# Optimization experiments

Measured on AMD Instinct MI355X. Metric: run time of the kernel, lower is better.

## Reference

```python
import jax, jax.numpy as jnp
import numpy as np

NEG_SLOPE = 0.2

def _gat_conv(x, src, dst, W, att_src, att_dst, bias, num_nodes):
    # x: [N, Fin], W: [H*C, Fin], att_*: [H, C], bias: [H*C]
    H, C = att_src.shape
    xh = (x @ W.T).reshape(num_nodes, H, C)            # [N,H,C]
    a_s = jnp.einsum('nhc,hc->nh', xh, att_src)         # [N,H]
    a_d = jnp.einsum('nhc,hc->nh', xh, att_dst)
    e = jax.nn.leaky_relu(a_s[src] + a_d[dst], NEG_SLOPE)  # [E,H]
    # segment softmax over destination node per head
    m = jax.ops.segment_max(e, dst, num_segments=num_nodes)      # [N,H]
    ex = jnp.exp(e - m[dst])
    s = jax.ops.segment_sum(ex, dst, num_segments=num_nodes)     # [N,H]
    alpha = ex / (s[dst] + 1e-16)                                # [E,H]
    msg = xh[src] * alpha[:, :, None]                            # [E,H,C]
    out = jax.ops.segment_sum(msg, dst, num_segments=num_nodes)  # [N,H,C]
    return out.reshape(num_nodes, H * C) + bias


def setup_inputs() -> dict:
    key = jax.random.key(0)
    ks = jax.random.split(key, 16)
    N, E, Fin, Hd, H1, G = 50000, 800000, 128, 128, 4, 128
    x = jax.random.normal(ks[0], (N, Fin), dtype=jnp.float32)
    edge_index = jax.random.randint(ks[1], (2, E), 0, N, dtype=jnp.int64)
    batch = jnp.sort(jax.random.randint(ks[2], (N,), 0, G, dtype=jnp.int64))
    sc1 = 1.0 / np.sqrt(Fin)
    sc2 = 1.0 / np.sqrt(Hd * H1)
    sch = 1.0 / np.sqrt(Hd)
    return {
        'x': x, 'edge_index': edge_index, 'batch': batch,
        'W1': jax.random.normal(ks[3], (Hd * H1, Fin), dtype=jnp.float32) * sc1,
        'as1': jax.random.normal(ks[4], (H1, Hd), dtype=jnp.float32) * 0.1,
        'ad1': jax.random.normal(ks[5], (H1, Hd), dtype=jnp.float32) * 0.1,
        'b1': jnp.zeros((Hd * H1,), dtype=jnp.float32),
        'W2': jax.random.normal(ks[6], (Hd, Hd * H1), dtype=jnp.float32) * sc2,
        'as2': jax.random.normal(ks[7], (1, Hd), dtype=jnp.float32) * 0.1,
        'ad2': jax.random.normal(ks[8], (1, Hd), dtype=jnp.float32) * 0.1,
        'b2': jnp.zeros((Hd,), dtype=jnp.float32),
        'Wh1': jax.random.normal(ks[9], (Hd, Hd), dtype=jnp.float32) * sch,
        'bh1': jnp.zeros((Hd,), dtype=jnp.float32),
        'Wh2': jax.random.normal(ks[10], (1, Hd), dtype=jnp.float32) * sch,
        'bh2': jnp.zeros((1,), dtype=jnp.float32),
    }


def reference(x, edge_index, batch, W1, as1, ad1, b1, W2, as2, ad2, b2, Wh1, bh1, Wh2, bh2):
    N = x.shape[0]
    G = 128  # num graphs
    # add self loops (PyG GATConv default)
    loops = jnp.arange(N, dtype=edge_index.dtype)
    src = jnp.concatenate([edge_index[0], loops])
    dst = jnp.concatenate([edge_index[1], loops])
    h = _gat_conv(x, src, dst, W1, as1, ad1, b1, N)   # [N, 512]
    h = jax.nn.elu(h)
    h = _gat_conv(h, src, dst, W2, as2, ad2, b2, N)   # [N, 128]
    h = jax.nn.elu(h)
    # global mean pool over batch
    sums = jax.ops.segment_sum(h, batch, num_segments=G)
    cnts = jax.ops.segment_sum(jnp.ones((N,), dtype=h.dtype), batch, num_segments=G)
    pooled = sums / jnp.maximum(cnts, 1.0)[:, None]   # [G, 128]
    z = jax.nn.relu(pooled @ Wh1.T + bh1)
    out = z @ Wh2.T + bh2                             # [G, 1]
    return out.reshape(-1)
```

## Files before the change

### kernel.cpp

```cpp
#include <hip/hip_runtime.h>
#include <cstdint>
#include <cstddef>

#define NEG_SLOPE 0.2f

typedef _Float16 f16x8 __attribute__((ext_vector_type(8)));
typedef _Float16 f16x2 __attribute__((ext_vector_type(2)));
typedef float    f32x4 __attribute__((ext_vector_type(4)));
typedef float    f32x2 __attribute__((ext_vector_type(2)));

__device__ __forceinline__ float leaky(float x){ return x > 0.f ? x : NEG_SLOPE * x; }
__device__ __forceinline__ float elu(float x){ return x > 0.f ? x : __expf(x) - 1.f; }

__global__ __launch_bounds__(256) void k_front(const float* __restrict__ W1,
                                               const float* __restrict__ W2,
                                               const float* __restrict__ as1,
                                               const float* __restrict__ ad1,
                                               _Float16* __restrict__ W1hi, _Float16* __restrict__ W1lo,
                                               _Float16* __restrict__ W2hi, _Float16* __restrict__ W2lo,
                                               float* __restrict__ w_s, float* __restrict__ w_d,
                                               const int* __restrict__ ei, int* __restrict__ deg,
                                               unsigned short* __restrict__ rank,
                                               const int* __restrict__ batch, int* __restrict__ gstart,
                                               int E, int Ep, int N, int G, int nbc)
{
    int b = blockIdx.x;
    if (b < 512) {
        const float* src = (b < 256) ? W1 : W2;
        _Float16* hi = (b < 256) ? W1hi : W2hi;
        _Float16* lo = (b < 256) ? W1lo : W2lo;
        int i = ((b & 255) << 8) + threadIdx.x;
        float v = src[i];
        _Float16 h = (_Float16)v;
        hi[i] = h;
        lo[i] = (_Float16)(v - (float)h);
    } else if (b < 514) {
        int h = (b - 512) * 2 + (threadIdx.x >> 7);
        int k = threadIdx.x & 127;
        float s = 0.f, d = 0.f;
        for (int c = 0; c < 128; ++c) {
            float w = W1[((size_t)(h * 128 + c)) * 128 + k];
            s += as1[h * 128 + c] * w;
            d += ad1[h * 128 + c] * w;
        }
        w_s[h * 128 + k] = s;
        w_d[h * 128 + k] = d;
    } else if (b < 514 + nbc) {
        int e = (b - 514) * 256 + threadIdx.x;
        if (e >= Ep) return;
        int dst = (e < E) ? ei[E + e] : (e - E);
        rank[e] = (unsigned short)atomicAdd(&deg[dst], 1);
    } else {
        int n = (b - 514 - nbc) * 256 + threadIdx.x;
        if (n >= N) return;
        int bb = batch[n];
        int prev = (n == 0) ? -1 : batch[n - 1];
        for (int g = prev + 1; g <= bb; ++g) gstart[g] = n;
        if (n == N - 1)
            for (int g = bb + 1; g <= G; ++g) gstart[g] = N;
    }
}

__global__ __launch_bounds__(1024) void k_scan_attn(const int* __restrict__ deg,
                                                    int* __restrict__ start,
                                                    int* __restrict__ sums,
                                                    int Ntot, int N, int nscan,
                                                    const float* __restrict__ x,
                                                    const float* __restrict__ w_s,
                                                    const float* __restrict__ w_d,
                                                    float* __restrict__ a_s,
                                                    float* __restrict__ a_d,
                                                    _Float16* __restrict__ xh)
{
    if ((int)blockIdx.x < nscan) {
        __shared__ int sm[1024];
        int tid = threadIdx.x;
        int i = blockIdx.x * 1024 + tid;
        int v = (i < N) ? deg[i] : 0;
        sm[tid] = v; __syncthreads();
        for (int off = 1; off < 1024; off <<= 1) {
            int t = (tid >= off) ? sm[tid - off] : 0;
            __syncthreads();
            sm[tid] += t;
            __syncthreads();
        }
        if (i < Ntot) start[i] = sm[tid] - v;
        if (tid == 1023) sums[blockIdx.x] = sm[1023];
    } else {
        int n = (blockIdx.x - nscan) * 16 + (threadIdx.x >> 6);
        if (n >= N) return;
        int lane = threadIdx.x & 63;
        float2 xv = *(const float2*)(x + (size_t)n * 128 + lane * 2);
        f16x2 hv = { (_Float16)xv.x, (_Float16)xv.y };
        *(f16x2*)(xh + (size_t)n * 128 + lane * 2) = hv;
        float ps[4], pd[4];
        #pragma unroll
        for (int h = 0; h < 4; ++h) {
            float2 sv = *(const float2*)(w_s + h * 128 + lane * 2);
            float2 dv = *(const float2*)(w_d + h * 128 + lane * 2);
            ps[h] = xv.x * sv.x + xv.y * sv.y;
            pd[h] = xv.x * dv.x + xv.y * dv.y;
        }
        #pragma unroll
        for (int h = 0; h < 4; ++h)
            for (int off = 32; off; off >>= 1) {
                ps[h] += __shfl_xor(ps[h], off);
                pd[h] += __shfl_xor(pd[h], off);
            }
        if (lane == 0) {
            *(float4*)(a_s + (size_t)n * 4) = make_float4(ps[0], ps[1], ps[2], ps[3]);
            *(float4*)(a_d + (size_t)n * 4) = make_float4(pd[0], pd[1], pd[2], pd[3]);
        }
    }
}

__global__ __launch_bounds__(1024) void k_scanC(int* __restrict__ start,
                                                const int* __restrict__ sums, int Ntot)
{
    int add = 0;
    for (int b = 0; b < (int)blockIdx.x; ++b) add += sums[b];
    int i = blockIdx.x * 1024 + threadIdx.x;
    if (i < Ntot) start[i] += add;
}

__global__ void k_fill(const int* __restrict__ ei, const int* __restrict__ start,
                       const unsigned short* __restrict__ rank,
                       unsigned short* __restrict__ csr_src, int E, int Ep)
{
    int e = blockIdx.x * blockDim.x + threadIdx.x;
    if (e >= Ep) return;
    int src, dst;
    if (e < E) { src = ei[e]; dst = ei[E + e]; } else { src = dst = e - E; }
    csr_src[start[dst] + rank[e]] = (unsigned short)src;
}

#define LSG 40
#define CP  136
__global__ __launch_bounds__(256, 2) void k_gemm12(
    const _Float16* __restrict__ agg,
    const _Float16* __restrict__ W1hi, const _Float16* __restrict__ W1lo,
    const float* __restrict__ b1,
    const _Float16* __restrict__ W2hi, const _Float16* __restrict__ W2lo,
    _Float16* __restrict__ xh2,
    const float* __restrict__ as2, const float* __restrict__ ad2,
    float* __restrict__ As2, float* __restrict__ Ad2, int M)
{
    __shared__ __align__(16) _Float16 smem[128 * LSG * 3 + 128 * CP];
    _Float16* As  = smem;
    _Float16* Bhs = smem + 128 * LSG;
    _Float16* Bls = smem + 256 * LSG;
    _Float16* Ct  = smem + 384 * LSG;

    const int tid = threadIdx.x;
    const int wave = tid >> 6, lane = tid & 63;
    const int wm = wave >> 1, wn = wave & 1;
    const int quad = lane >> 4, l16 = lane & 15;
    const int m0 = blockIdx.x * 128;

    f32x4 acc2[4][4] = {};

    for (int h = 0; h < 4; ++h) {
        f32x4 acc1[4][4] = {};
        for (int k0 = 0; k0 < 128; k0 += 32) {
            #pragma unroll
            for (int q = 0; q < 2; ++q) {
                int idx = tid + q * 256;
                int row = idx >> 2, kq = idx & 3;
                int rg = m0 + row;
                f16x8 va = {};
                if (rg < M) va = *(const f16x8*)(agg + (size_t)rg * 512 + h * 128 + k0 + kq * 8);
                *(f16x8*)&As[row * LSG + kq * 8] = va;
                size_t brow = (size_t)(h * 128 + row) * 128 + k0 + kq * 8;
                *(f16x8*)&Bhs[row * LSG + kq * 8] = *(const f16x8*)(W1hi + brow);
                *(f16x8*)&Bls[row * LSG + kq * 8] = *(const f16x8*)(W1lo + brow);
            }
            __syncthreads();
            f16x8 af[4], bhf[4], blf[4];
            #pragma unroll
            for (int i = 0; i < 4; ++i) {
                af[i]  = *(const f16x8*)&As [(wm * 64 + i * 16 + l16) * LSG + quad * 8];
                bhf[i] = *(const f16x8*)&Bhs[(wn * 64 + i * 16 + l16) * LSG + quad * 8];
                blf[i] = *(const f16x8*)&Bls[(wn * 64 + i * 16 + l16) * LSG + quad * 8];
            }
            #pragma unroll
            for (int i = 0; i < 4; ++i)
                #pragma unroll
                for (int j = 0; j < 4; ++j) {
                    acc1[i][j] = __builtin_amdgcn_mfma_f32_16x16x32_f16(af[i], bhf[j], acc1[i][j], 0, 0, 0);
                    acc1[i][j] = __builtin_amdgcn_mfma_f32_16x16x32_f16(af[i], blf[j], acc1[i][j], 0, 0, 0);
                }
            __syncthreads();
        }
        #pragma unroll
        for (int j = 0; j < 4; ++j) {
            int n = wn * 64 + j * 16 + l16;
            float bb = b1[h * 128 + n];
            #pragma unroll
            for (int i = 0; i < 4; ++i)
                #pragma unroll
                for (int r = 0; r < 4; ++r)
                    Ct[(wm * 64 + i * 16 + quad * 4 + r) * CP + n] = (_Float16)elu(acc1[i][j][r] + bb);
        }
        __syncthreads();
        for (int k0 = 0; k0 < 128; k0 += 32) {
            #pragma unroll
            for (int q = 0; q < 2; ++q) {
                int idx = tid + q * 256;
                int row = idx >> 2, kq = idx & 3;
                size_t brow = (size_t)row * 512 + h * 128 + k0 + kq * 8;
                *(f16x8*)&Bhs[row * LSG + kq * 8] = *(const f16x8*)(W2hi + brow);
                *(f16x8*)&Bls[row * LSG + kq * 8] = *(const f16x8*)(W2lo + brow);
            }
            __syncthreads();
            f16x8 af[4], bhf[4], blf[4];
            #pragma unroll
            for (int i = 0; i < 4; ++i) {
                af[i]  = *(const f16x8*)&Ct [(wm * 64 + i * 16 + l16) * CP + k0 + quad * 8];
                bhf[i] = *(const f16x8*)&Bhs[(wn * 64 + i * 16 + l16) * LSG + quad * 8];
                blf[i] = *(const f16x8*)&Bls[(wn * 64 + i * 16 + l16) * LSG + quad * 8];
            }
            #pragma unroll
            for (int i = 0; i < 4; ++i)
                #pragma unroll
                for (int j = 0; j < 4; ++j) {
                    acc2[i][j] = __builtin_amdgcn_mfma_f32_16x16x32_f16(af[i], bhf[j], acc2[i][j], 0, 0, 0);
                    acc2[i][j] = __builtin_amdgcn_mfma_f32_16x16x32_f16(af[i], blf[j], acc2[i][j], 0, 0, 0);
                }
            __syncthreads();
        }
    }

    #pragma unroll
    for (int j = 0; j < 4; ++j) {
        int n = wn * 64 + j * 16 + l16;
        #pragma unroll
        for (int i = 0; i < 4; ++i)
            #pragma unroll
            for (int r = 0; r < 4; ++r)
                Ct[(wm * 64 + i * 16 + quad * 4 + r) * CP + n] = (_Float16)acc2[i][j][r];
    }
    __syncthreads();
    for (int c = tid; c < 2048; c += 256) {
        int row = c >> 4, col8 = (c & 15) * 8;
        int m = m0 + row;
        if (m < M)
            *(f16x8*)(xh2 + (size_t)m * 128 + col8) = *(const f16x8*)&Ct[row * CP + col8];
    }
    {
        int row = tid >> 1, half = tid & 1;
        int d = m0 + row;
        float ss = 0.f, sd = 0.f;
        const _Float16* rp = &Ct[row * CP + half * 64];
        #pragma unroll
        for (int c8 = 0; c8 < 8; ++c8) {
            f16x8 v = *(const f16x8*)(rp + c8 * 8);
            #pragma unroll
            for (int c = 0; c < 8; ++c) {
                float f = (float)v[c];
                int n = half * 64 + c8 * 8 + c;
                ss += f * as2[n];
                sd += f * ad2[n];
            }
        }
        ss += __shfl_xor(ss, 1);
        sd += __shfl_xor(sd, 1);
        if (half == 0 && d < M) { As2[d] = ss; Ad2[d] = sd; }
    }
}

__global__ __launch_bounds__(256) void k_gat1(const int* __restrict__ start,
                                              const unsigned short* __restrict__ csr,
                                              const float* __restrict__ a_s,
                                              const float* __restrict__ a_d,
                                              const _Float16* __restrict__ x,
                                              _Float16* __restrict__ agg, int N)
{
    int d = blockIdx.x * 16 + (threadIdx.x >> 4);
    if (d >= N) return;
    int g16 = threadIdx.x & 15;
    int beg = start[d], end = start[d + 1];
    int deg = end - beg;
    float4 ad4 = *(const float4*)(a_d + (size_t)d * 4);

    float sum0 = 0.f, sum1 = 0.f, sum2 = 0.f, sum3 = 0.f;
    f32x2 acc[4][4] = {};
    const _Float16* xb = x + g16 * 8;

    for (int base = 0; base < deg; base += 16) {
        int nch = deg - base; if (nch > 16) nch = 16;
        int s = 0;
        float e0 = 0.f, e1 = 0.f, e2 = 0.f, e3 = 0.f;
        if (g16 < nch) {
            s = csr[beg + base + g16];
            float4 as4 = *(const float4*)(a_s + (size_t)s * 4);
            e0 = __expf(leaky(as4.x + ad4.x));
            e1 = __expf(leaky(as4.y + ad4.y));
            e2 = __expf(leaky(as4.z + ad4.z));
            e3 = __expf(leaky(as4.w + ad4.w));
            sum0 += e0; sum1 += e1; sum2 += e2; sum3 += e3;
        }
        int t = 0;
        for (; t + 8 <= nch; t += 8) {
            int si[8];
            #pragma unroll
            for (int u = 0; u < 8; ++u) si[u] = __shfl(s, t + u, 16);
            f16x8 hv[8];
            #pragma unroll
            for (int u = 0; u < 8; ++u) hv[u] = *(const f16x8*)(xb + (size_t)si[u] * 128);
            #pragma unroll
            for (int u = 0; u < 8; ++u) {
                float w0 = __shfl(e0, t + u, 16), w1 = __shfl(e1, t + u, 16);
                float w2 = __shfl(e2, t + u, 16), w3 = __shfl(e3, t + u, 16);
                #pragma unroll
                for (int p = 0; p < 4; ++p) {
                    f32x2 v = { (float)hv[u][2*p], (float)hv[u][2*p+1] };
                    acc[0][p] += w0 * v;
                    acc[1][p] += w1 * v;
                    acc[2][p] += w2 * v;
                    acc[3][p] += w3 * v;
                }
            }
        }
        for (; t + 4 <= nch; t += 4) {
            int sA = __shfl(s, t, 16),     sB = __shfl(s, t + 1, 16);
            int sC = __shfl(s, t + 2, 16), sD = __shfl(s, t + 3, 16);
            f16x8 hA = *(const f16x8*)(xb + (size_t)sA * 128);
            f16x8 hB = *(const f16x8*)(xb + (size_t)sB * 128);
            f16x8 hC = *(const f16x8*)(xb + (size_t)sC * 128);
            f16x8 hD = *(const f16x8*)(xb + (size_t)sD * 128);
            float w0A = __shfl(e0, t, 16),     w1A = __shfl(e1, t, 16);
            float w2A = __shfl(e2, t, 16),     w3A = __shfl(e3, t, 16);
            float w0B = __shfl(e0, t + 1, 16), w1B = __shfl(e1, t + 1, 16);
            float w2B = __shfl(e2, t + 1, 16), w3B = __shfl(e3, t + 1, 16);
            float w0C = __shfl(e0, t + 2, 16), w1C = __shfl(e1, t + 2, 16);
            float w2C = __shfl(e2, t + 2, 16), w3C = __shfl(e3, t + 2, 16);
            float w0D = __shfl(e0, t + 3, 16), w1D = __shfl(e1, t + 3, 16);
            float w2D = __shfl(e2, t + 3, 16), w3D = __shfl(e3, t + 3, 16);
            #pragma unroll
            for (int p = 0; p < 4; ++p) {
                f32x2 vA = { (float)hA[2*p], (float)hA[2*p+1] };
                f32x2 vB = { (float)hB[2*p], (float)hB[2*p+1] };
                f32x2 vC = { (float)hC[2*p], (float)hC[2*p+1] };
                f32x2 vD = { (float)hD[2*p], (float)hD[2*p+1] };
                acc[0][p] += w0A * vA + w0B * vB + w0C * vC + w0D * vD;
                acc[1][p] += w1A * vA + w1B * vB + w1C * vC + w1D * vD;
                acc[2][p] += w2A * vA + w2B * vB + w2C * vC + w2D * vD;
                acc[3][p] += w3A * vA + w3B * vB + w3C * vC + w3D * vD;
            }
        }
        for (; t < nch; ++t) {
            int   si = __shfl(s,  t, 16);
            float w0 = __shfl(e0, t, 16);
            float w1 = __shfl(e1, t, 16);
            float w2 = __shfl(e2, t, 16);
            float w3 = __shfl(e3, t, 16);
            f16x8 hv = *(const f16x8*)(xb + (size_t)si * 128);
            #pragma unroll
            for (int p = 0; p < 4; ++p) {
                f32x2 v = { (float)hv[2*p], (float)hv[2*p+1] };
                acc[0][p] += w0 * v;
                acc[1][p] += w1 * v;
                acc[2][p] += w2 * v;
                acc[3][p] += w3 * v;
            }
        }
    }
    #pragma unroll
    for (int o = 1; o < 16; o <<= 1) {
        sum0 += __shfl_xor(sum0, o, 16); sum1 += __shfl_xor(sum1, o, 16);
        sum2 += __shfl_xor(sum2, o, 16); sum3 += __shfl_xor(sum3, o, 16);
    }
    float inv[4] = { 1.f / (sum0 + 1e-16f), 1.f / (sum1 + 1e-16f),
                     1.f / (sum2 + 1e-16f), 1.f / (sum3 + 1e-16f) };
    _Float16* o = agg + (size_t)d * 512 + g16 * 8;
    #pragma unroll
    for (int h = 0; h < 4; ++h) {
        f16x8 ov;
        #pragma unroll
        for (int p = 0; p < 4; ++p) {
            ov[2 * p]     = (_Float16)(acc[h][p].x * inv[h]);
            ov[2 * p + 1] = (_Float16)(acc[h][p].y * inv[h]);
        }
        *(f16x8*)(o + h * 128) = ov;
    }
}

__global__ __launch_bounds__(256) void k_gat2(const int* __restrict__ start,
                                              const unsigned short* __restrict__ csr,
                                              const float* __restrict__ a_s,
                                              const float* __restrict__ a_d,
                                              const _Float16* __restrict__ xh2,
                                              const float* __restrict__ b2,
                                              const int* __restrict__ batch,
                                              float* __restrict__ pooled, int N)
{
    __shared__ float sm[16][128];
    __shared__ int sbat[16];
    const int grp = threadIdx.x >> 4;
    const int g16 = threadIdx.x & 15;
    const int d = blockIdx.x * 16 + grp;

    float vals[8];
    #pragma unroll
    for (int j = 0; j < 8; ++j) vals[j] = 0.f;

    if (d < N) {
        int beg = start[d], end = start[d + 1];
        int deg = end - beg;
        float ad = a_d[d];
        float sum = 0.f;
        f32x2 acc[4] = {};
        const _Float16* xb = xh2 + g16 * 8;

        for (int base = 0; base < deg; base += 16) {
            int nch = deg - base; if (nch > 16) nch = 16;
            int s = 0; float e = 0.f;
            if (g16 < nch) {
                s = csr[beg + base + g16];
                e = __expf(leaky(a_s[s] + ad));
                sum += e;
            }
            int t = 0;
            for (; t + 8 <= nch; t += 8) {
                int si[8];
                #pragma unroll
                for (int u = 0; u < 8; ++u) si[u] = __shfl(s, t + u, 16);
                f16x8 hv[8];
                #pragma unroll
                for (int u = 0; u < 8; ++u) hv[u] = *(const f16x8*)(xb + (size_t)si[u] * 128);
                #pragma unroll
                for (int u = 0; u < 8; ++u) {
                    float w = __shfl(e, t + u, 16);
                    #pragma unroll
                    for (int p = 0; p < 4; ++p) {
                        f32x2 v = { (float)hv[u][2*p], (float)hv[u][2*p+1] };
                        acc[p] += w * v;
                    }
                }
            }
            for (; t + 4 <= nch; t += 4) {
                int sA = __shfl(s, t, 16),     sB = __shfl(s, t + 1, 16);
                int sC = __shfl(s, t + 2, 16), sD = __shfl(s, t + 3, 16);
                f16x8 hA = *(const f16x8*)(xb + (size_t)sA * 128);
                f16x8 hB = *(const f16x8*)(xb + (size_t)sB * 128);
                f16x8 hC = *(const f16x8*)(xb + (size_t)sC * 128);
                f16x8 hD = *(const f16x8*)(xb + (size_t)sD * 128);
                float wA = __shfl(e, t, 16),     wB = __shfl(e, t + 1, 16);
                float wC = __shfl(e, t + 2, 16), wD = __shfl(e, t + 3, 16);
                #pragma unroll
                for (int p = 0; p < 4; ++p) {
                    f32x2 vA = { (float)hA[2*p], (float)hA[2*p+1] };
                    f32x2 vB = { (float)hB[2*p], (float)hB[2*p+1] };
                    f32x2 vC = { (float)hC[2*p], (float)hC[2*p+1] };
                    f32x2 vD = { (float)hD[2*p], (float)hD[2*p+1] };
                    acc[p] += wA * vA + wB * vB + wC * vC + wD * vD;
                }
            }
            for (; t < nch; ++t) {
                int   si = __shfl(s, t, 16);
                float w  = __shfl(e, t, 16);
                f16x8 hv = *(const f16x8*)(xb + (size_t)si * 128);
                #pragma unroll
                for (int p = 0; p < 4; ++p) {
                    f32x2 v = { (float)hv[2*p], (float)hv[2*p+1] };
                    acc[p] += w * v;
                }
            }
        }
        #pragma unroll
        for (int o = 1; o < 16; o <<= 1) sum += __shfl_xor(sum, o, 16);
        float inv = 1.f / (sum + 1e-16f);
        #pragma unroll
        for (int p = 0; p < 4; ++p) {
            vals[2 * p]     = elu(acc[p].x * inv + b2[g16 * 8 + 2 * p]);
            vals[2 * p + 1] = elu(acc[p].y * inv + b2[g16 * 8 + 2 * p + 1]);
        }
        if (g16 == 0) sbat[grp] = batch[d];
    } else {
        if (g16 == 0) sbat[grp] = -1;
    }
    #pragma unroll
    for (int j = 0; j < 8; ++j) sm[grp][g16 * 8 + j] = vals[j];
    __syncthreads();

    if (threadIdx.x < 128) {
        int c = threadIdx.x;
        float acc = 0.f;
        int g = sbat[0];
        #pragma unroll
        for (int r = 0; r < 16; ++r) {
            int bg = sbat[r];
            if (bg < 0) break;
            if (bg != g) { atomicAdd(&pooled[(size_t)g * 128 + c], acc); acc = 0.f; g = bg; }
            acc += sm[r][c];
        }
        atomicAdd(&pooled[(size_t)g * 128 + c], acc);
    }
}

__global__ __launch_bounds__(128) void k_head(const float* __restrict__ pooled,
                                              const int* __restrict__ gstart,
                                              const float* __restrict__ Wh1,
                                              const float* __restrict__ bh1,
                                              const float* __restrict__ Wh2,
                                              const float* __restrict__ bh2,
                                              float* __restrict__ out)
{
    int g = blockIdx.x, c = threadIdx.x;
    __shared__ float p[128];
    __shared__ float red[128];
    float cf = (float)(gstart[g + 1] - gstart[g]); cf = cf > 1.f ? cf : 1.f;
    p[c] = pooled[(size_t)g * 128 + c] / cf;
    __syncthreads();
    float z = bh1[c];
    for (int k = 0; k < 128; ++k) z += p[k] * Wh1[c * 128 + k];
    z = z > 0.f ? z : 0.f;
    red[c] = z * Wh2[c];
    __syncthreads();
    for (int st = 64; st > 0; st >>= 1) { if (c < st) red[c] += red[c + st]; __syncthreads(); }
    if (c == 0) out[g] = red[0] + bh2[0];
}

extern "C" void kernel_launch(void* const* d_in, const int* in_sizes, int n_in,
                              void* d_out, int out_size, void* d_ws, size_t ws_size,
                              hipStream_t stream)
{
    const float* x   = (const float*)d_in[0];
    const int*   ei  = (const int*)d_in[1];
    const int*   bat = (const int*)d_in[2];
    const float* W1  = (const float*)d_in[3];
    const float* as1 = (const float*)d_in[4];
    const float* ad1 = (const float*)d_in[5];
    const float* b1  = (const float*)d_in[6];
    const float* W2  = (const float*)d_in[7];
    const float* as2 = (const float*)d_in[8];
    const float* ad2 = (const float*)d_in[9];
    const float* b2  = (const float*)d_in[10];
    const float* Wh1 = (const float*)d_in[11];
    const float* bh1 = (const float*)d_in[12];
    const float* Wh2 = (const float*)d_in[13];
    const float* bh2 = (const float*)d_in[14];
    float* out = (float*)d_out;

    const int N  = in_sizes[0] / 128;
    const int E  = in_sizes[1] / 2;
    const int Ep = E + N;
    const int G  = 128;
    const int nscan = (N + 1 + 1023) / 1024;

    char* w = (char*)d_ws;
    size_t off = 0;
    auto alloc = [&](size_t bytes) -> char* {
        char* p = w + off; off += (bytes + 511) & ~(size_t)511; return p;
    };
    _Float16* x_h  = (_Float16*)alloc((size_t)N * 128 * 2);
    _Float16* agg  = (_Float16*)alloc((size_t)N * 512 * 2);
    _Float16* xh2h = (_Float16*)alloc((size_t)N * 128 * 2);
    float*    As1  = (float*)alloc((size_t)N * 4 * 4);
    float*    Ad1  = (float*)alloc((size_t)N * 4 * 4);
    float*    As2  = (float*)alloc((size_t)N * 4);
    float*    Ad2  = (float*)alloc((size_t)N * 4);
    float*    w_s1 = (float*)alloc(512 * 4);
    float*    w_d1 = (float*)alloc(512 * 4);
    _Float16* W1hi = (_Float16*)alloc(65536 * 2);
    _Float16* W1lo = (_Float16*)alloc(65536 * 2);
    _Float16* W2hi = (_Float16*)alloc(65536 * 2);
    _Float16* W2lo = (_Float16*)alloc(65536 * 2);
    int* startb = (int*)alloc((size_t)(N + 1) * 4);
    unsigned short* csr  = (unsigned short*)alloc((size_t)Ep * 2);
    unsigned short* rank = (unsigned short*)alloc((size_t)Ep * 2);
    int* sums   = (int*)alloc(4096);
    int* gstart = (int*)alloc((size_t)(G + 1) * 4);
    char* zbase = w + off;
    int*   deg    = (int*)alloc((size_t)N * 4);
    float* pooled = (float*)alloc((size_t)G * 128 * 4);
    size_t zbytes = (size_t)((w + off) - zbase);

    hipMemsetAsync(zbase, 0, zbytes, stream);

    int nbc = (Ep + 255) / 256, nbg = (N + 255) / 256;
    k_front<<<514 + nbc + nbg, 256, 0, stream>>>(W1, W2, as1, ad1, W1hi, W1lo, W2hi, W2lo,
                                                 w_s1, w_d1, ei, deg, rank, bat, gstart,
                                                 E, Ep, N, G, nbc);
    k_scan_attn<<<nscan + (N + 15) / 16, 1024, 0, stream>>>(deg, startb, sums, N + 1, N, nscan,
                                                            x, w_s1, w_d1, As1, Ad1, x_h);
    k_scanC<<<nscan, 1024, 0, stream>>>(startb, sums, N + 1);
    k_fill<<<(Ep + 255) / 256, 256, 0, stream>>>(ei, startb, rank, csr, E, Ep);
    k_gat1<<<(N + 15) / 16, 256, 0, stream>>>(startb, csr, As1, Ad1, x_h, agg, N);
    k_gemm12<<<(N + 127) / 128, 256, 0, stream>>>(agg, W1hi, W1lo, b1, W2hi, W2lo,
                                                  xh2h, as2, ad2, As2, Ad2, N);
    k_gat2<<<(N + 15) / 16, 256, 0, stream>>>(startb, csr, As2, Ad2, xh2h, b2, bat, pooled, N);
    k_head<<<G, 128, 0, stream>>>(pooled, gstart, Wh1, bh1, Wh2, bh2, out);
}
```

Baseline: 311.9 us.

## Software-pipeline fused two-layer GEMM with register prefetch of next K tile

```diff
diff --git a/kernel.cpp b/kernel.cpp
--- a/kernel.cpp
+++ b/kernel.cpp
@@ -158,30 +158,68 @@
     const int m0 = blockIdx.x * 128;
 
     f32x4 acc2[4][4] = {};
-
-    for (int h = 0; h < 4; ++h) {
-        f32x4 acc1[4][4] = {};
-        for (int k0 = 0; k0 < 128; k0 += 32) {
+    f32x4 acc1[4][4];
+    f16x8 rA[2], rBh[2], rBl[2];
+
+    auto issue = [&](int step) {
+        int head = step >> 3, sub = step & 7, k0 = (sub & 3) * 32;
+        if (sub < 4) {
             #pragma unroll
             for (int q = 0; q < 2; ++q) {
-                int idx = tid + q * 256;
-                int row = idx >> 2, kq = idx & 3;
+                int idx = tid + q * 256, row = idx >> 2, kq = idx & 3;
                 int rg = m0 + row;
                 f16x8 va = {};
-                if (rg < M) va = *(const f16x8*)(agg + (size_t)rg * 512 + h * 128 + k0 + kq * 8);
-                *(f16x8*)&As[row * LSG + kq * 8] = va;
-                size_t brow = (size_t)(h * 128 + row) * 128 + k0 + kq * 8;
-                *(f16x8*)&Bhs[row * LSG + kq * 8] = *(const f16x8*)(W1hi + brow);
-                *(f16x8*)&Bls[row * LSG + kq * 8] = *(const f16x8*)(W1lo + brow);
-            }
-            __syncthreads();
-            f16x8 af[4], bhf[4], blf[4];
-            #pragma unroll
-            for (int i = 0; i < 4; ++i) {
-                af[i]  = *(const f16x8*)&As [(wm * 64 + i * 16 + l16) * LSG + quad * 8];
-                bhf[i] = *(const f16x8*)&Bhs[(wn * 64 + i * 16 + l16) * LSG + quad * 8];
-                blf[i] = *(const f16x8*)&Bls[(wn * 64 + i * 16 + l16) * LSG + quad * 8];
-            }
+                if (rg < M) va = *(const f16x8*)(agg + (size_t)rg * 512 + head * 128 + k0 + kq * 8);
+                rA[q] = va;
+                size_t brow = (size_t)(head * 128 + row) * 128 + k0 + kq * 8;
+                rBh[q] = *(const f16x8*)(W1hi + brow);
+                rBl[q] = *(const f16x8*)(W1lo + brow);
+            }
+        } else {
+            #pragma unroll
+            for (int q = 0; q < 2; ++q) {
+                int idx = tid + q * 256, row = idx >> 2, kq = idx & 3;
+                size_t brow = (size_t)row * 512 + head * 128 + k0 + kq * 8;
+                rBh[q] = *(const f16x8*)(W2hi + brow);
+                rBl[q] = *(const f16x8*)(W2lo + brow);
+            }
+        }
+    };
+
+    issue(0);
+
+    for (int step = 0; step < 32; ++step) {
+        const int head = step >> 3, sub = step & 7;
+        const int st2 = sub >> 2, k0 = (sub & 3) * 32;
+
+        if (sub == 0) {
+            #pragma unroll
+            for (int i = 0; i < 4; ++i)
+                #pragma unroll
+                for (int j = 0; j < 4; ++j)
+                    acc1[i][j] = (f32x4){};
+        }
+
+        __syncthreads();
+        #pragma unroll
+        for (int q = 0; q < 2; ++q) {
+            int idx = tid + q * 256, row = idx >> 2, kq = idx & 3;
+            if (!st2) *(f16x8*)&As[row * LSG + kq * 8] = rA[q];
+            *(f16x8*)&Bhs[row * LSG + kq * 8] = rBh[q];
+            *(f16x8*)&Bls[row * LSG + kq * 8] = rBl[q];
+        }
+        if (step + 1 < 32) issue(step + 1);
+        __syncthreads();
+
+        f16x8 af[4], bhf[4], blf[4];
+        #pragma unroll
+        for (int i = 0; i < 4; ++i) {
+            if (!st2) af[i] = *(const f16x8*)&As[(wm * 64 + i * 16 + l16) * LSG + quad * 8];
+            else      af[i] = *(const f16x8*)&Ct[(wm * 64 + i * 16 + l16) * CP + k0 + quad * 8];
+            bhf[i] = *(const f16x8*)&Bhs[(wn * 64 + i * 16 + l16) * LSG + quad * 8];
+            blf[i] = *(const f16x8*)&Bls[(wn * 64 + i * 16 + l16) * LSG + quad * 8];
+        }
+        if (!st2) {
             #pragma unroll
             for (int i = 0; i < 4; ++i)
                 #pragma unroll
@@ -189,36 +227,7 @@
                     acc1[i][j] = __builtin_amdgcn_mfma_f32_16x16x32_f16(af[i], bhf[j], acc1[i][j], 0, 0, 0);
                     acc1[i][j] = __builtin_amdgcn_mfma_f32_16x16x32_f16(af[i], blf[j], acc1[i][j], 0, 0, 0);
                 }
-            __syncthreads();
-        }
-        #pragma unroll
-        for (int j = 0; j < 4; ++j) {
-            int n = wn * 64 + j * 16 + l16;
-            float bb = b1[h * 128 + n];
-            #pragma unroll
-            for (int i = 0; i < 4; ++i)
-                #pragma unroll
-                for (int r = 0; r < 4; ++r)
-                    Ct[(wm * 64 + i * 16 + quad * 4 + r) * CP + n] = (_Float16)elu(acc1[i][j][r] + bb);
-        }
-        __syncthreads();
-        for (int k0 = 0; k0 < 128; k0 += 32) {
-            #pragma unroll
-            for (int q = 0; q < 2; ++q) {
-                int idx = tid + q * 256;
-                int row = idx >> 2, kq = idx & 3;
-                size_t brow = (size_t)row * 512 + h * 128 + k0 + kq * 8;
-                *(f16x8*)&Bhs[row * LSG + kq * 8] = *(const f16x8*)(W2hi + brow);
-                *(f16x8*)&Bls[row * LSG + kq * 8] = *(const f16x8*)(W2lo + brow);
-            }
-            __syncthreads();
-            f16x8 af[4], bhf[4], blf[4];
-            #pragma unroll
-            for (int i = 0; i < 4; ++i) {
-                af[i]  = *(const f16x8*)&Ct [(wm * 64 + i * 16 + l16) * CP + k0 + quad * 8];
-                bhf[i] = *(const f16x8*)&Bhs[(wn * 64 + i * 16 + l16) * LSG + quad * 8];
-                blf[i] = *(const f16x8*)&Bls[(wn * 64 + i * 16 + l16) * LSG + quad * 8];
-            }
+        } else {
             #pragma unroll
             for (int i = 0; i < 4; ++i)
                 #pragma unroll
@@ -226,10 +235,23 @@
                     acc2[i][j] = __builtin_amdgcn_mfma_f32_16x16x32_f16(af[i], bhf[j], acc2[i][j], 0, 0, 0);
                     acc2[i][j] = __builtin_amdgcn_mfma_f32_16x16x32_f16(af[i], blf[j], acc2[i][j], 0, 0, 0);
                 }
-            __syncthreads();
-        }
-    }
-
+        }
+
+        if (sub == 3) {
+            #pragma unroll
+            for (int j = 0; j < 4; ++j) {
+                int n = wn * 64 + j * 16 + l16;
+                float bb = b1[head * 128 + n];
+                #pragma unroll
+                for (int i = 0; i < 4; ++i)
+                    #pragma unroll
+                    for (int r = 0; r < 4; ++r)
+                        Ct[(wm * 64 + i * 16 + quad * 4 + r) * CP + n] = (_Float16)elu(acc1[i][j][r] + bb);
+            }
+        }
+    }
+
+    __syncthreads();
     #pragma unroll
     for (int j = 0; j < 4; ++j) {
         int n = wn * 64 + j * 16 + l16;
```

Result: slower. 363.9 us (+16.7%).
